# Performance work log

Hardware: AMD Instinct MI355X
Metric: run time of the kernel (lower is better)

Reference implementation:

```python
import jax, jax.numpy as jnp
import numpy as np

B, S, H = 2, 2048, 1024
NH, HD = 16, 64
ROPE_BASE = 10000.0


def setup_inputs() -> dict:
    key = jax.random.key(0)
    ks = jax.random.split(key, 8)
    sc = 1.0 / np.sqrt(H)
    return {
        "hidden_states": jax.random.normal(ks[0], (B, S, H), dtype=jnp.float32),
        "position_ids": jnp.arange(S, dtype=jnp.int64 if jax.config.jax_enable_x64 else jnp.int32)[None, :],
        "Wq": jax.random.normal(ks[1], (H, H), dtype=jnp.float32) * sc,
        "bq": jax.random.normal(ks[2], (H,), dtype=jnp.float32) * 0.02,
        "Wk": jax.random.normal(ks[3], (H, H), dtype=jnp.float32) * sc,
        "bk": jax.random.normal(ks[4], (H,), dtype=jnp.float32) * 0.02,
        "Wv": jax.random.normal(ks[5], (H, H), dtype=jnp.float32) * sc,
        "bv": jax.random.normal(ks[6], (H,), dtype=jnp.float32) * 0.02,
        "Wo": jax.random.normal(ks[7], (H, H), dtype=jnp.float32) * sc,
    }


def _rotate_half(x):
    x1, x2 = x[..., : HD // 2], x[..., HD // 2:]
    return jnp.concatenate((-x2, x1), axis=-1)


def _rope_tables(seq_len, dtype):
    inv_freq = 1.0 / (ROPE_BASE ** (jnp.arange(0, HD, 2, dtype=jnp.float32) / HD))
    t = jnp.arange(seq_len, dtype=jnp.float32)
    freqs = jnp.einsum("s,d->sd", t, inv_freq)          # [S, HD/2]
    emb = jnp.concatenate((freqs, freqs), axis=-1)       # [S, HD]
    return jnp.cos(emb).astype(dtype), jnp.sin(emb).astype(dtype)


def reference(hidden_states, position_ids, Wq, bq, Wk, bk, Wv, bv, Wo):
    bsz, q_len, _ = hidden_states.shape
    # QKV projections (torch Linear: x @ W.T + b)
    q = (hidden_states @ Wq.T + bq).reshape(bsz, q_len, NH, HD).transpose(0, 2, 1, 3)
    k = (hidden_states @ Wk.T + bk).reshape(bsz, q_len, NH, HD).transpose(0, 2, 1, 3)
    v = (hidden_states @ Wv.T + bv).reshape(bsz, q_len, NH, HD).transpose(0, 2, 1, 3)
    # RoPE
    cos, sin = _rope_tables(q_len, hidden_states.dtype)
    cos = cos[position_ids][:, None]  # [1, 1, S, HD] (unsqueeze_dim=1)
    sin = sin[position_ids][:, None]
    q = q * cos + _rotate_half(q) * sin
    k = k * cos + _rotate_half(k) * sin
    # scaled dot-product attention (mask=None, dropout=0)
    scale = 1.0 / jnp.sqrt(jnp.asarray(HD, hidden_states.dtype))
    scores = jnp.einsum("bhqd,bhkd->bhqk", q, k) * scale
    probs = jax.nn.softmax(scores, axis=-1)
    attn = jnp.einsum("bhqk,bhkd->bhqd", probs, v)
    attn = attn.transpose(0, 2, 1, 3).reshape(bsz, q_len, H)
    return attn @ Wo.T
```

## Files before the change

### kernel.cpp

```cpp
#include <hip/hip_runtime.h>
#include <hip/hip_bf16.h>
#include <math.h>

#define SS 2048
#define HH 1024
#define NHH 16
#define HDD 64
#define BH 32
#define MM 4096

typedef unsigned short u16;
using bf16x8 = __attribute__((ext_vector_type(8))) short;
using floatx4 = __attribute__((ext_vector_type(4))) float;

__device__ __forceinline__ u16 f2bf(float f) {
  unsigned u = __float_as_uint(f);
  u += 0x7fffu + ((u >> 16) & 1u);
  return (u16)(u >> 16);
}
__device__ __forceinline__ unsigned pk_bf16(float a, float b) {
  union { __hip_bfloat162 h2; unsigned u; } c;
  c.h2 = __float22bfloat162_rn(float2{a, b});
  return c.u;
}
__device__ __forceinline__ void gload_lds16(const u16* g, u16* l) {
  __builtin_amdgcn_global_load_lds(
      (const __attribute__((address_space(1))) void*)g,
      (__attribute__((address_space(3))) void*)l, 16, 0, 0);
}

__global__ __launch_bounds__(256) void convert_bf(
    const float* __restrict__ hs, const float* __restrict__ wq,
    const float* __restrict__ wk, const float* __restrict__ wv,
    const float* __restrict__ wo, const int* __restrict__ pos,
    u16* __restrict__ hs_b, u16* __restrict__ wq_b, u16* __restrict__ wk_b,
    u16* __restrict__ wv_b, u16* __restrict__ wo_b,
    float2* __restrict__ tab) {
  int g = blockIdx.x * 256 + threadIdx.x;
  if (g < 2097152) {
    const float* src;
    u16* dst;
    int off;
    if (g < 1048576) {
      src = hs; dst = hs_b; off = g;
    } else {
      int t = g - 1048576;
      int w = t >> 18;
      off = t & 262143;
      src = (w == 0) ? wq : (w == 1) ? wk : (w == 2) ? wv : wo;
      dst = (w == 0) ? wq_b : (w == 1) ? wk_b : (w == 2) ? wv_b : wo_b;
    }
    float4 v = ((const float4*)src)[off];
    ushort4 o = make_ushort4(f2bf(v.x), f2bf(v.y), f2bf(v.z), f2bf(v.w));
    ((ushort4*)dst)[off] = o;
  } else {
    int idx = g - 2097152;
    int s = idx >> 5, j = idx & 31;
    float p = (float)pos[s];
    const float c0 = 13.287712379549449f / 32.0f;
    float f = p * exp2f(-(float)j * c0);
    float sn, cs;
    sincosf(f, &sn, &cs);
    tab[idx] = float2{cs, sn};
  }
}

__global__ __launch_bounds__(256) void mfma_gemm_qkv(
    const u16* __restrict__ X, const u16* __restrict__ W0,
    const u16* __restrict__ W1, const u16* __restrict__ W2,
    const float* __restrict__ b0, const float* __restrict__ b1,
    const float* __restrict__ b2, const float2* __restrict__ tab,
    u16* __restrict__ O0, u16* __restrict__ O1, u16* __restrict__ O2) {
  __shared__ __align__(16) u16 As[128 * 32];
  __shared__ __align__(16) u16 Bs[128 * 32];
  const int tid = threadIdx.x;
  const int lane = tid & 63;
  const int wvu = __builtin_amdgcn_readfirstlane(tid >> 6);
  const int l15 = lane & 15;
  const int quad = lane >> 4;
  const int wm = wvu >> 1, wn = wvu & 1;
  const int m0 = blockIdx.y * 128;
  const int n0g = blockIdx.x * 128;
  const int lr = lane >> 2;
  const int lc = lane & 3;

  int wsel = n0g >> 10;
  int n0 = n0g & 1023;
  const u16* Wsel = (wsel == 1) ? W1 : (wsel == 2) ? W2 : W0;
  const float* bsel = (wsel == 1) ? b1 : (wsel == 2) ? b2 : b0;
  u16* Osel = (wsel == 1) ? O1 : (wsel == 2) ? O2 : O0;

  floatx4 acc[4][4];
#pragma unroll
  for (int i = 0; i < 4; ++i)
#pragma unroll
    for (int j = 0; j < 4; ++j) acc[i][j] = (floatx4){0.f, 0.f, 0.f, 0.f};

  const int scol = (lc ^ ((lr >> 1) & 3)) * 8;
  const int fsw = ((l15 >> 1) & 3);

  for (int k0 = 0; k0 < HH; k0 += 32) {
#pragma unroll
    for (int u = 0; u < 2; ++u) {
      int r = u * 64 + wvu * 16 + lr;
      gload_lds16(&X[(size_t)(m0 + r) * HH + k0 + scol],
                  &As[(u * 64 + wvu * 16) * 32]);
      gload_lds16(&Wsel[(size_t)(n0 + r) * HH + k0 + scol],
                  &Bs[(u * 64 + wvu * 16) * 32]);
    }
    __syncthreads();
    bf16x8 af[4], bfr[4];
#pragma unroll
    for (int mb = 0; mb < 4; ++mb)
      af[mb] = *(const bf16x8*)&As[(wm * 64 + mb * 16 + l15) * 32 +
                                   ((quad ^ fsw) * 8)];
#pragma unroll
    for (int nb = 0; nb < 4; ++nb)
      bfr[nb] = *(const bf16x8*)&Bs[(wn * 64 + nb * 16 + l15) * 32 +
                                    ((quad ^ fsw) * 8)];
#pragma unroll
    for (int mb = 0; mb < 4; ++mb)
#pragma unroll
      for (int nb = 0; nb < 4; ++nb)
        acc[mb][nb] = __builtin_amdgcn_mfma_f32_16x16x32_bf16(
            af[mb], bfr[nb], acc[mb][nb], 0, 0, 0);
    __syncthreads();
  }

  if (wsel < 2) {
    const float qs = (wsel == 0) ? 0.125f * 1.44269504088896f : 1.0f;
    const int colb = n0 + wn * 64;
    const int h = colb >> 6;
    const float bias0 = bsel[colb + l15];
    const float bias1 = bsel[colb + 16 + l15];
    const float bias2 = bsel[colb + 32 + l15];
    const float bias3 = bsel[colb + 48 + l15];
#pragma unroll
    for (int mb = 0; mb < 4; ++mb)
#pragma unroll
      for (int r = 0; r < 4; ++r) {
        int m = m0 + wm * 64 + mb * 16 + quad * 4 + r;
        int b = m >> 11, s = m & (SS - 1);
        float2 t0 = tab[s * 32 + l15];
        float2 t1 = tab[s * 32 + 16 + l15];
        size_t obase = ((size_t)(b * NHH + h) * SS + s) * HDD;
        float x1 = acc[mb][0][r] + bias0;
        float x2 = acc[mb][2][r] + bias2;
        Osel[obase + l15] = f2bf((x1 * t0.x - x2 * t0.y) * qs);
        Osel[obase + 32 + l15] = f2bf((x2 * t0.x + x1 * t0.y) * qs);
        float y1 = acc[mb][1][r] + bias1;
        float y2 = acc[mb][3][r] + bias3;
        Osel[obase + 16 + l15] = f2bf((y1 * t1.x - y2 * t1.y) * qs);
        Osel[obase + 48 + l15] = f2bf((y2 * t1.x + y1 * t1.y) * qs);
      }
  } else {
#pragma unroll
    for (int nb = 0; nb < 4; ++nb) {
      int col = n0 + wn * 64 + nb * 16 + l15;
      int h = col >> 6, d = col & 63;
      float bias = bsel[col];
#pragma unroll
      for (int mb = 0; mb < 4; ++mb) {
        int m = m0 + wm * 64 + mb * 16 + quad * 4;
        int b = m >> 11, s = m & (SS - 1);
        uint2 w2;
        w2.x = pk_bf16(acc[mb][nb][0] + bias, acc[mb][nb][1] + bias);
        w2.y = pk_bf16(acc[mb][nb][2] + bias, acc[mb][nb][3] + bias);
        *(uint2*)&Osel[((size_t)((b * NHH + h) * HDD + d)) * SS + s] = w2;
      }
    }
  }
}

__global__ __launch_bounds__(256) void gemm_out(const u16* __restrict__ X,
                                                const u16* __restrict__ W,
                                                float* __restrict__ Ofp) {
  __shared__ __align__(16) u16 As[128 * 32];
  __shared__ __align__(16) u16 Bs[64 * 32];
  const int tid = threadIdx.x;
  const int lane = tid & 63;
  const int wvu = __builtin_amdgcn_readfirstlane(tid >> 6);
  const int l15 = lane & 15;
  const int quad = lane >> 4;
  const int wm = wvu >> 1, wn = wvu & 1;
  const int m0 = blockIdx.y * 128;
  const int n0 = blockIdx.x * 64;
  const int lr = lane >> 2;
  const int lc = lane & 3;

  floatx4 acc[4][2];
#pragma unroll
  for (int i = 0; i < 4; ++i)
#pragma unroll
    for (int j = 0; j < 2; ++j) acc[i][j] = (floatx4){0.f, 0.f, 0.f, 0.f};

  const int scol = (lc ^ ((lr >> 1) & 3)) * 8;
  const int fsw = ((l15 >> 1) & 3);

  for (int k0 = 0; k0 < HH; k0 += 32) {
#pragma unroll
    for (int u = 0; u < 2; ++u) {
      int r = u * 64 + wvu * 16 + lr;
      gload_lds16(&X[(size_t)(m0 + r) * HH + k0 + scol],
                  &As[(u * 64 + wvu * 16) * 32]);
    }
    gload_lds16(&W[(size_t)(n0 + wvu * 16 + lr) * HH + k0 + scol],
                &Bs[(wvu * 16) * 32]);
    __syncthreads();
    bf16x8 af[4], bfr[2];
#pragma unroll
    for (int mb = 0; mb < 4; ++mb)
      af[mb] = *(const bf16x8*)&As[(wm * 64 + mb * 16 + l15) * 32 +
                                   ((quad ^ fsw) * 8)];
#pragma unroll
    for (int nb = 0; nb < 2; ++nb)
      bfr[nb] = *(const bf16x8*)&Bs[(wn * 32 + nb * 16 + l15) * 32 +
                                    ((quad ^ fsw) * 8)];
#pragma unroll
    for (int mb = 0; mb < 4; ++mb)
#pragma unroll
      for (int nb = 0; nb < 2; ++nb)
        acc[mb][nb] = __builtin_amdgcn_mfma_f32_16x16x32_bf16(
            af[mb], bfr[nb], acc[mb][nb], 0, 0, 0);
    __syncthreads();
  }

#pragma unroll
  for (int mb = 0; mb < 4; ++mb)
#pragma unroll
    for (int r = 0; r < 4; ++r) {
      int m = m0 + wm * 64 + mb * 16 + quad * 4 + r;
#pragma unroll
      for (int nb = 0; nb < 2; ++nb)
        Ofp[(size_t)m * HH + n0 + wn * 32 + nb * 16 + l15] = acc[mb][nb][r];
    }
}

__global__ __launch_bounds__(256, 4) void attn_mfma(const u16* __restrict__ Qg,
                                                    const u16* __restrict__ Kg,
                                                    const u16* __restrict__ Vtg,
                                                    u16* __restrict__ A) {
  __shared__ __align__(16) u16 smem[16384];
  u16* const Ks0 = smem;
  u16* const Ks1 = smem + 4096;
  u16* const Vs0 = smem + 8192;
  u16* const Vs1 = smem + 12288;
  float* const lpart = (float*)smem;
  float* const Opart = (float*)smem + 128;

  const int tid = threadIdx.x;
  const int lane = tid & 63;
  const int wv = __builtin_amdgcn_readfirstlane(tid >> 6);
  const int l15 = lane & 15, quad = lane >> 4;
  const int sw7 = l15 & 7;
  const int bh = blockIdx.x, qt = blockIdx.y;
  const size_t hb = (size_t)bh * SS * HDD;
  const int kh = wv >> 1;
  const int qh = wv & 1;

  const int r8 = lane >> 3, c7 = lane & 7;
  const int cs = (c7 ^ r8) * 8;
  const u16* kgb[2];
  const u16* vgb[2];
#pragma unroll
  for (int u = 0; u < 2; ++u) {
    int row = (wv * 2 + u) * 8 + r8;
    kgb[u] = Kg + hb + (size_t)row * HDD + cs;
    vgb[u] = Vtg + hb + (size_t)row * SS + cs;
  }

#pragma unroll
  for (int u = 0; u < 2; ++u) {
    int row = (wv * 2 + u) * 8 + r8;
    gload_lds16(&Qg[hb + (size_t)(qt * 64 + row) * HDD + cs],
                Ks1 + (wv * 2 + u) * 512);
    gload_lds16(kgb[u], Ks0 + (wv * 2 + u) * 512);
    gload_lds16(vgb[u], Vs0 + (wv * 2 + u) * 512);
  }
  __syncthreads();

  bf16x8 qf[2][2];
#pragma unroll
  for (int nb = 0; nb < 2; ++nb)
#pragma unroll
    for (int h2 = 0; h2 < 2; ++h2)
      qf[nb][h2] = *(const bf16x8*)&Ks1[(qh * 32 + nb * 16 + l15) * 64 +
                                        (((h2 * 4 + quad) ^ sw7) * 8)];
  __syncthreads();

  float l_acc[2] = {0.f, 0.f};
  floatx4 o[4][2];
#pragma unroll
  for (int dmb = 0; dmb < 4; ++dmb)
#pragma unroll
    for (int nb = 0; nb < 2; ++nb) o[dmb][nb] = (floatx4){0.f, 0.f, 0.f, 0.f};

  for (int t = 0; t < SS / 64; ++t) {
    if (t + 1 < SS / 64) {
      u16* kd = ((t + 1) & 1) ? Ks1 : Ks0;
      u16* vd = ((t + 1) & 1) ? Vs1 : Vs0;
#pragma unroll
      for (int u = 0; u < 2; ++u) {
        gload_lds16(kgb[u] + (size_t)(t + 1) * 64 * HDD,
                    kd + (wv * 2 + u) * 512);
        gload_lds16(vgb[u] + (t + 1) * 64, vd + (wv * 2 + u) * 512);
      }
    }
    const u16* ks = (t & 1) ? Ks1 : Ks0;
    const u16* vs = (t & 1) ? Vs1 : Vs0;

    floatx4 st[2][2];
#pragma unroll
    for (int kmb = 0; kmb < 2; ++kmb) {
      int krow = kh * 32 + kmb * 16 + l15;
      bf16x8 ak0 = *(const bf16x8*)&ks[krow * 64 + ((quad ^ sw7) * 8)];
      bf16x8 ak1 = *(const bf16x8*)&ks[krow * 64 + (((4 + quad) ^ sw7) * 8)];
#pragma unroll
      for (int nb = 0; nb < 2; ++nb) {
        floatx4 z = (floatx4){0.f, 0.f, 0.f, 0.f};
        z = __builtin_amdgcn_mfma_f32_16x16x32_bf16(ak0, qf[nb][0], z, 0, 0, 0);
        z = __builtin_amdgcn_mfma_f32_16x16x32_bf16(ak1, qf[nb][1], z, 0, 0, 0);
        st[kmb][nb] = z;
      }
    }

    bf16x8 bp[2];
#pragma unroll
    for (int nb = 0; nb < 2; ++nb) {
      float p00 = exp2f(st[0][nb][0]), p01 = exp2f(st[0][nb][1]);
      float p02 = exp2f(st[0][nb][2]), p03 = exp2f(st[0][nb][3]);
      float p10 = exp2f(st[1][nb][0]), p11 = exp2f(st[1][nb][1]);
      float p12 = exp2f(st[1][nb][2]), p13 = exp2f(st[1][nb][3]);
      l_acc[nb] += ((p00 + p01) + (p02 + p03)) + ((p10 + p11) + (p12 + p13));
      union { bf16x8 v; unsigned u[4]; } pu;
      pu.u[0] = pk_bf16(p00, p01);
      pu.u[1] = pk_bf16(p02, p03);
      pu.u[2] = pk_bf16(p10, p11);
      pu.u[3] = pk_bf16(p12, p13);
      bp[nb] = pu.v;
    }

    const int cb0 = kh * 4 + (quad >> 1);
    const int cb1 = cb0 + 2;
    const int sub = (quad & 1) * 4;
#pragma unroll
    for (int dmb = 0; dmb < 4; ++dmb) {
      int vr = (dmb * 16 + l15) * 64;
      union { bf16x8 v; uint2 d2[2]; } au;
      au.d2[0] = *(const uint2*)&vs[vr + ((cb0 ^ sw7) * 8) + sub];
      au.d2[1] = *(const uint2*)&vs[vr + ((cb1 ^ sw7) * 8) + sub];
#pragma unroll
      for (int nb = 0; nb < 2; ++nb)
        o[dmb][nb] = __builtin_amdgcn_mfma_f32_16x16x32_bf16(au.v, bp[nb],
                                                             o[dmb][nb], 0, 0, 0);
    }
    __syncthreads();
  }

#pragma unroll
  for (int nb = 0; nb < 2; ++nb) {
    l_acc[nb] += __shfl_xor(l_acc[nb], 16);
    l_acc[nb] += __shfl_xor(l_acc[nb], 32);
  }
  if (quad == 0) {
    lpart[wv * 32 + l15] = l_acc[0];
    lpart[wv * 32 + 16 + l15] = l_acc[1];
  }
  if (kh == 1) {
    float* dst = Opart + qh * (32 * 68);
#pragma unroll
    for (int nb = 0; nb < 2; ++nb)
#pragma unroll
      for (int dmb = 0; dmb < 4; ++dmb)
        *(floatx4*)&dst[(nb * 16 + l15) * 68 + dmb * 16 + quad * 4] =
            o[dmb][nb];
  }
  __syncthreads();
  if (kh == 0) {
    const int b = bh >> 4, h = bh & 15;
    const float* src = Opart + qh * (32 * 68);
    float inv[2];
#pragma unroll
    for (int nb = 0; nb < 2; ++nb)
      inv[nb] = 1.f / (lpart[wv * 32 + nb * 16 + l15] +
                       lpart[(wv + 2) * 32 + nb * 16 + l15]);
#pragma unroll
    for (int nb = 0; nb < 2; ++nb) {
      int s = qt * 64 + qh * 32 + nb * 16 + l15;
#pragma unroll
      for (int dmb = 0; dmb < 4; ++dmb) {
        floatx4 part =
            *(const floatx4*)&src[(nb * 16 + l15) * 68 + dmb * 16 + quad * 4];
        floatx4 tot = (o[dmb][nb] + part) * inv[nb];
        uint2 w2;
        w2.x = pk_bf16(tot[0], tot[1]);
        w2.y = pk_bf16(tot[2], tot[3]);
        *(uint2*)&A[((size_t)(b * SS + s) * HH) + h * HDD + dmb * 16 +
                    quad * 4] = w2;
      }
    }
  }
}

extern "C" void kernel_launch(void* const* d_in, const int* in_sizes, int n_in,
                              void* d_out, int out_size, void* d_ws,
                              size_t ws_size, hipStream_t stream) {
  const float* hs = (const float*)d_in[0];
  const int* pos = (const int*)d_in[1];
  const float* Wq = (const float*)d_in[2];
  const float* bq = (const float*)d_in[3];
  const float* Wk = (const float*)d_in[4];
  const float* bk = (const float*)d_in[5];
  const float* Wv = (const float*)d_in[6];
  const float* bv = (const float*)d_in[7];
  const float* Wo = (const float*)d_in[8];
  float* out = (float*)d_out;

  u16* hs_b = (u16*)d_ws;
  u16* wq_b = hs_b + 4194304;
  u16* wk_b = wq_b + 1048576;
  u16* wv_b = wk_b + 1048576;
  u16* wo_b = wv_b + 1048576;
  u16* Qb = wo_b + 1048576;
  u16* Kb = Qb + 4194304;
  u16* Vtb = Kb + 4194304;
  u16* Ab = Vtb + 4194304;
  float2* tab = (float2*)(Ab + 4194304);

  hipLaunchKernelGGL(convert_bf, dim3(8448), dim3(256), 0, stream, hs, Wq, Wk,
                     Wv, Wo, pos, hs_b, wq_b, wk_b, wv_b, wo_b, tab);
  hipLaunchKernelGGL(mfma_gemm_qkv, dim3(24, 32), dim3(256), 0, stream, hs_b,
                     wq_b, wk_b, wv_b, bq, bk, bv, tab, Qb, Kb, Vtb);
  hipLaunchKernelGGL(attn_mfma, dim3(32, 32), dim3(256), 0, stream, Qb, Kb,
                     Vtb, Ab);
  hipLaunchKernelGGL(gemm_out, dim3(16, 32), dim3(256), 0, stream, Ab, wo_b,
                     out);
}
```

Before: 217.6 us.

## Load K directly to registers and give each wave private V buffers without block barriers

Q and K fragments are now read straight from global memory into registers, with K for the next tile prefetched into registers. Each wave keeps its own double-buffered V slice in LDS, so the per-iteration __syncthreads is replaced by a waitcnt. The grid axes are swapped so q-tiles of the same head are launched next to each other, and launch bounds drop from 4 to 3 waves per SIMD to leave room for more registers. The aim is to cut barrier stalls and LDS traffic for K, at the cost of higher register pressure, lower occupancy and uncoalesced 16-byte global loads for K.

```diff
diff --git a/kernel.cpp b/kernel.cpp
--- a/kernel.cpp
+++ b/kernel.cpp
@@ -236,57 +236,48 @@
     }
 }
 
-__global__ __launch_bounds__(256, 4) void attn_mfma(const u16* __restrict__ Qg,
+__global__ __launch_bounds__(256, 3) void attn_mfma(const u16* __restrict__ Qg,
                                                     const u16* __restrict__ Kg,
                                                     const u16* __restrict__ Vtg,
                                                     u16* __restrict__ A) {
   __shared__ __align__(16) u16 smem[16384];
-  u16* const Ks0 = smem;
-  u16* const Ks1 = smem + 4096;
-  u16* const Vs0 = smem + 8192;
-  u16* const Vs1 = smem + 12288;
-  float* const lpart = (float*)smem;
-  float* const Opart = (float*)smem + 128;
-
   const int tid = threadIdx.x;
   const int lane = tid & 63;
   const int wv = __builtin_amdgcn_readfirstlane(tid >> 6);
   const int l15 = lane & 15, quad = lane >> 4;
-  const int sw7 = l15 & 7;
-  const int bh = blockIdx.x, qt = blockIdx.y;
+  const int qt = blockIdx.x, bh = blockIdx.y;
   const size_t hb = (size_t)bh * SS * HDD;
-  const int kh = wv >> 1;
-  const int qh = wv & 1;
-
-  const int r8 = lane >> 3, c7 = lane & 7;
-  const int cs = (c7 ^ r8) * 8;
-  const u16* kgb[2];
-  const u16* vgb[2];
-#pragma unroll
-  for (int u = 0; u < 2; ++u) {
-    int row = (wv * 2 + u) * 8 + r8;
-    kgb[u] = Kg + hb + (size_t)row * HDD + cs;
-    vgb[u] = Vtg + hb + (size_t)row * SS + cs;
-  }
-
-#pragma unroll
-  for (int u = 0; u < 2; ++u) {
-    int row = (wv * 2 + u) * 8 + r8;
-    gload_lds16(&Qg[hb + (size_t)(qt * 64 + row) * HDD + cs],
-                Ks1 + (wv * 2 + u) * 512);
-    gload_lds16(kgb[u], Ks0 + (wv * 2 + u) * 512);
-    gload_lds16(vgb[u], Vs0 + (wv * 2 + u) * 512);
-  }
-  __syncthreads();
+  const int kh = wv >> 1, qh = wv & 1;
+
+  u16* const vbuf0 = smem + wv * 2048;
+  u16* const vbuf1 = smem + 8192 + wv * 2048;
+
+  const int r4 = lane >> 2, c4 = lane & 3;
+  const u16* vsrc =
+      Vtg + hb + (size_t)r4 * SS + kh * 32 + ((c4 ^ (r4 & 3)) * 8);
 
   bf16x8 qf[2][2];
 #pragma unroll
   for (int nb = 0; nb < 2; ++nb)
 #pragma unroll
-    for (int h2 = 0; h2 < 2; ++h2)
-      qf[nb][h2] = *(const bf16x8*)&Ks1[(qh * 32 + nb * 16 + l15) * 64 +
-                                        (((h2 * 4 + quad) ^ sw7) * 8)];
-  __syncthreads();
+    for (int ch = 0; ch < 2; ++ch)
+      qf[nb][ch] = *(const bf16x8*)&Qg[hb +
+                                       (size_t)(qt * 64 + qh * 32 + nb * 16 +
+                                                l15) *
+                                           HDD +
+                                       ch * 32 + quad * 8];
+
+  const u16* kbase = Kg + hb + (size_t)(kh * 32 + l15) * HDD + quad * 8;
+  bf16x8 kf[2][2];
+#pragma unroll
+  for (int kmb = 0; kmb < 2; ++kmb)
+#pragma unroll
+    for (int ch = 0; ch < 2; ++ch)
+      kf[kmb][ch] = *(const bf16x8*)&kbase[(size_t)(kmb * 16) * HDD + ch * 32];
+
+#pragma unroll
+  for (int u = 0; u < 4; ++u)
+    gload_lds16(vsrc + (size_t)(u * 16) * SS, vbuf0 + u * 512);
 
   float l_acc[2] = {0.f, 0.f};
   floatx4 o[4][2];
@@ -295,34 +286,53 @@
 #pragma unroll
     for (int nb = 0; nb < 2; ++nb) o[dmb][nb] = (floatx4){0.f, 0.f, 0.f, 0.f};
 
+  const int sub = (quad & 1) * 4;
+  const int sx = l15 & 3;
+  const int vc0 = ((quad >> 1) ^ sx) * 8 + sub;
+  const int vc1 = (((quad >> 1) + 2) ^ sx) * 8 + sub;
+
   for (int t = 0; t < SS / 64; ++t) {
-    if (t + 1 < SS / 64) {
-      u16* kd = ((t + 1) & 1) ? Ks1 : Ks0;
-      u16* vd = ((t + 1) & 1) ? Vs1 : Vs0;
-#pragma unroll
-      for (int u = 0; u < 2; ++u) {
-        gload_lds16(kgb[u] + (size_t)(t + 1) * 64 * HDD,
-                    kd + (wv * 2 + u) * 512);
-        gload_lds16(vgb[u] + (t + 1) * 64, vd + (wv * 2 + u) * 512);
-      }
-    }
-    const u16* ks = (t & 1) ? Ks1 : Ks0;
-    const u16* vs = (t & 1) ? Vs1 : Vs0;
+    __builtin_amdgcn_s_waitcnt(0);
+    const u16* vb = (t & 1) ? vbuf1 : vbuf0;
+
+    bf16x8 au[4];
+#pragma unroll
+    for (int dmb = 0; dmb < 4; ++dmb) {
+      int rb = (dmb * 16 + l15) * 32;
+      union { bf16x8 v; uint2 d2[2]; } c;
+      c.d2[0] = *(const uint2*)&vb[rb + vc0];
+      c.d2[1] = *(const uint2*)&vb[rb + vc1];
+      au[dmb] = c.v;
+    }
+
+    const int tn = (t + 1 < SS / 64) ? t + 1 : t;
+    {
+      u16* vd = (t & 1) ? vbuf0 : vbuf1;
+#pragma unroll
+      for (int u = 0; u < 4; ++u)
+        gload_lds16(vsrc + (size_t)(u * 16) * SS + tn * 64, vd + u * 512);
+    }
+    bf16x8 kn[2][2];
+#pragma unroll
+    for (int kmb = 0; kmb < 2; ++kmb)
+#pragma unroll
+      for (int ch = 0; ch < 2; ++ch)
+        kn[kmb][ch] = *(const bf16x8*)&kbase[(size_t)(tn * 64 + kmb * 16) *
+                                                 HDD +
+                                             ch * 32];
 
     floatx4 st[2][2];
 #pragma unroll
-    for (int kmb = 0; kmb < 2; ++kmb) {
-      int krow = kh * 32 + kmb * 16 + l15;
-      bf16x8 ak0 = *(const bf16x8*)&ks[krow * 64 + ((quad ^ sw7) * 8)];
-      bf16x8 ak1 = *(const bf16x8*)&ks[krow * 64 + (((4 + quad) ^ sw7) * 8)];
+    for (int kmb = 0; kmb < 2; ++kmb)
 #pragma unroll
       for (int nb = 0; nb < 2; ++nb) {
         floatx4 z = (floatx4){0.f, 0.f, 0.f, 0.f};
-        z = __builtin_amdgcn_mfma_f32_16x16x32_bf16(ak0, qf[nb][0], z, 0, 0, 0);
-        z = __builtin_amdgcn_mfma_f32_16x16x32_bf16(ak1, qf[nb][1], z, 0, 0, 0);
+        z = __builtin_amdgcn_mfma_f32_16x16x32_bf16(kf[kmb][0], qf[nb][0], z,
+                                                    0, 0, 0);
+        z = __builtin_amdgcn_mfma_f32_16x16x32_bf16(kf[kmb][1], qf[nb][1], z,
+                                                    0, 0, 0);
         st[kmb][nb] = z;
       }
-    }
 
     bf16x8 bp[2];
 #pragma unroll
@@ -340,22 +350,22 @@
       bp[nb] = pu.v;
     }
 
-    const int cb0 = kh * 4 + (quad >> 1);
-    const int cb1 = cb0 + 2;
-    const int sub = (quad & 1) * 4;
-#pragma unroll
-    for (int dmb = 0; dmb < 4; ++dmb) {
-      int vr = (dmb * 16 + l15) * 64;
-      union { bf16x8 v; uint2 d2[2]; } au;
-      au.d2[0] = *(const uint2*)&vs[vr + ((cb0 ^ sw7) * 8) + sub];
-      au.d2[1] = *(const uint2*)&vs[vr + ((cb1 ^ sw7) * 8) + sub];
+#pragma unroll
+    for (int dmb = 0; dmb < 4; ++dmb)
 #pragma unroll
       for (int nb = 0; nb < 2; ++nb)
-        o[dmb][nb] = __builtin_amdgcn_mfma_f32_16x16x32_bf16(au.v, bp[nb],
-                                                             o[dmb][nb], 0, 0, 0);
-    }
-    __syncthreads();
-  }
+        o[dmb][nb] = __builtin_amdgcn_mfma_f32_16x16x32_bf16(
+            au[dmb], bp[nb], o[dmb][nb], 0, 0, 0);
+
+#pragma unroll
+    for (int kmb = 0; kmb < 2; ++kmb)
+#pragma unroll
+      for (int ch = 0; ch < 2; ++ch) kf[kmb][ch] = kn[kmb][ch];
+  }
+
+  __syncthreads();
+  float* const lpart = (float*)smem;
+  float* const Opart = (float*)smem + 128;
 
 #pragma unroll
   for (int nb = 0; nb < 2; ++nb) {
```

Result: slower. 241.5 us (+11.0%).
